# Kernel tuning notes

Measured on AMD Instinct MI355X. Metric: run time of the kernel, lower is better.

## Reference

```python
import jax, jax.numpy as jnp
import numpy as np
from jax import lax

B, CHI, CHO, H, W = 8, 128, 128, 64, 64
K = 3
KK = K * K


def setup_inputs() -> dict:
    key = jax.random.key(0)
    ks = jax.random.split(key, 7)
    x = jax.random.normal(ks[0], (B, CHI, H, W), jnp.float32)
    # small offset-conv weights so sampled offsets stay in a realistic few-pixel range
    off_w = jax.random.normal(ks[1], (3 * KK, CHI, K, K), jnp.float32) * 0.01
    off_b = jnp.zeros((3 * KK,), jnp.float32)
    w = jax.random.normal(ks[2], (CHO, CHI, K, K), jnp.float32) / np.sqrt(CHI * KK).astype(np.float32)
    b = jnp.zeros((CHO,), jnp.float32)
    gamma = jax.random.uniform(ks[3], (CHO,), jnp.float32)  # nn.init.uniform_ on BN weight
    beta = jnp.zeros((CHO,), jnp.float32)
    return {"x": x, "off_w": off_w, "off_b": off_b, "w": w, "b": b, "gamma": gamma, "beta": beta}


def _deform_conv(x, off_w, off_b, w, b):
    """DCNv2 modulated deformable conv, k=3, stride=1, pad=1, dil=1, 1 deform group."""
    B_, C, H_, W_ = x.shape
    # offset/mask branch: plain 3x3 conv -> 27 channels (2*9 offsets, 9 masks)
    om = lax.conv_general_dilated(x, off_w, (1, 1), ((1, 1), (1, 1)),
                                  dimension_numbers=("NCHW", "OIHW", "NCHW"))
    om = om + off_b[None, :, None, None]
    off = om[:, : 2 * KK].reshape(B_, KK, 2, H_, W_)  # [B,9,2,H,W]; ch 2k=y, 2k+1=x
    mask = jax.nn.sigmoid(om[:, 2 * KK:])             # [B,9,H,W]

    ky, kx = jnp.meshgrid(jnp.arange(K, dtype=jnp.float32),
                          jnp.arange(K, dtype=jnp.float32), indexing="ij")
    ky = ky.reshape(KK); kx = kx.reshape(KK)
    # sampling positions: p = p0 - pad + k*dil + offset
    py = off[:, :, 0] + (jnp.arange(H_, dtype=jnp.float32) - 1.0)[None, None, :, None] + ky[None, :, None, None]
    px = off[:, :, 1] + (jnp.arange(W_, dtype=jnp.float32) - 1.0)[None, None, None, :] + kx[None, :, None, None]

    y0 = jnp.floor(py); x0 = jnp.floor(px)
    ly = py - y0; lx = px - x0
    xf = x.reshape(B_, C, H_ * W_)

    def corner(yi, xi, wgt):
        valid = ((yi >= 0) & (yi <= H_ - 1) & (xi >= 0) & (xi <= W_ - 1)).astype(x.dtype)
        yc = jnp.clip(yi, 0, H_ - 1).astype(jnp.int32)
        xc = jnp.clip(xi, 0, W_ - 1).astype(jnp.int32)
        idx = (yc * W_ + xc).reshape(B_, KK * H_ * W_)
        g = jax.vmap(lambda xb, ib: xb[:, ib])(xf, idx).reshape(B_, C, KK, H_, W_)
        return g * (valid * wgt)[:, None]

    val = (corner(y0, x0, (1 - ly) * (1 - lx))
           + corner(y0, x0 + 1, (1 - ly) * lx)
           + corner(y0 + 1, x0, ly * (1 - lx))
           + corner(y0 + 1, x0 + 1, ly * lx))  # [B,C,9,H,W]
    val = val * mask[:, None]  # modulation
    out = jnp.einsum("bckhw,ock->bohw", val, w.reshape(w.shape[0], C, KK))
    return out + b[None, :, None, None]


def reference(x, off_w, off_b, w, b, gamma, beta):
    y = _deform_conv(x, off_w, off_b, w, b)
    # BatchNorm2d in training mode (batch statistics), eps=1e-5, then ReLU
    mean = y.mean(axis=(0, 2, 3))
    var = y.var(axis=(0, 2, 3))
    yn = (y - mean[None, :, None, None]) * lax.rsqrt(var[None, :, None, None] + 1e-5)
    return jax.nn.relu(yn * gamma[None, :, None, None] + beta[None, :, None, None])
```

## Files before the change

### kernel.cpp

```cpp
#include <hip/hip_runtime.h>
#include <hip/hip_bf16.h>
#include <math.h>

#define HH 64
#define WW 64
#define HW 4096
#define LDV 136

typedef __bf16 bf16x8 __attribute__((ext_vector_type(8)));
typedef float floatx4 __attribute__((ext_vector_type(4)));
typedef unsigned int uint4a __attribute__((ext_vector_type(4)));
typedef unsigned int uint2a __attribute__((ext_vector_type(2)));

#define WS_Y    0u
#define WS_PSQ  16777216u
#define WS_XTB  16778240u
#define WS_WTB  25166848u
#define WS_OWB  25461760u

static __device__ inline ushort f2bf(float f) {
  __hip_bfloat16 h = __float2bfloat16(f);
  return __builtin_bit_cast(ushort, h);
}
static __device__ inline float lo16(unsigned int u) { return __builtin_bit_cast(float, u << 16); }
static __device__ inline float hi16(unsigned int u) { return __builtin_bit_cast(float, u & 0xffff0000u); }

static __device__ inline void barrier_lds() {
  asm volatile("s_waitcnt lgkmcnt(0)" ::: "memory");
  __builtin_amdgcn_s_barrier();
}

__global__ __launch_bounds__(256) void k_prep(const float* __restrict__ x,
                                              const float* __restrict__ w,
                                              const float* __restrict__ ow,
                                              ushort* __restrict__ xtb,
                                              ushort* __restrict__ wtb,
                                              ushort* __restrict__ owb,
                                              float* __restrict__ psq) {
  __shared__ float tile[32][33];
  int bid = blockIdx.x;
  if (bid < 4096) {
    int hw0 = (bid & 127) * 32;
    int c0 = ((bid >> 7) & 3) * 32;
    int b = bid >> 9;
    int col = threadIdx.x & 31, row = threadIdx.x >> 5;
    const float* xb = x + ((size_t)b * 128 + c0) * HW + hw0;
#pragma unroll
    for (int i = 0; i < 32; i += 8)
      tile[row + i][col] = xb[(size_t)(row + i) * HW + col];
    __syncthreads();
    int hw = threadIdx.x >> 3, cq = threadIdx.x & 7;
    ushort* xo = xtb + ((size_t)b * HW + hw0) * 128 + c0;
    unsigned int lo = (unsigned int)f2bf(tile[cq * 4 + 0][hw]) |
                      ((unsigned int)f2bf(tile[cq * 4 + 1][hw]) << 16);
    unsigned int hi = (unsigned int)f2bf(tile[cq * 4 + 2][hw]) |
                      ((unsigned int)f2bf(tile[cq * 4 + 3][hw]) << 16);
    uint2a v2 = (uint2a){lo, hi};
    *(uint2a*)(&xo[(size_t)hw * 128 + cq * 4]) = v2;
  } else if (bid < 4096 + 576) {
    int idx = (bid - 4096) * 256 + threadIdx.x;
    int c = idx & 127, o = (idx >> 7) & 127, k = idx >> 14;
    wtb[idx] = f2bf(w[(o * 128 + c) * 9 + k]);
  } else if (bid < 4096 + 720) {
    int j = (bid - 4672) * 256 + threadIdx.x;
    int c = j & 127, o = (j >> 7) & 31, k = j >> 12;
    float v = (o < 27) ? ow[(o * 128 + c) * 9 + k] : 0.f;
    owb[j] = f2bf(v);
  } else {
    psq[threadIdx.x] = 0.f;
  }
}

__global__ __launch_bounds__(256) void k_main(
    const ushort* __restrict__ xtb, const ushort* __restrict__ wtb,
    const ushort* __restrict__ owb, const float* __restrict__ off_b,
    const float* __restrict__ bias, float* __restrict__ y) {
  __shared__ ushort Vl[2][32 * LDV];
  __shared__ float omL[27 * 32];
  int t = threadIdx.x;
  int lane = t & 63, wv = t >> 6;
  int li = lane & 15, quad = lane >> 4;
  int hr = blockIdx.x;
  int row = hr >> 1, p0b = (hr & 1) * 32;
  int b = blockIdx.y;
  const ushort* xb = xtb + (size_t)b * HW * 128;
  int ch = t & 15;
  int pq = t >> 4;

  int mi = wv & 1, ni = wv >> 1;
  floatx4 oacc = (floatx4){0.f, 0.f, 0.f, 0.f};
  uint4a u0, u1;
  auto p1load = [&](int k, int p, uint4a& u) {
    int ky = k / 3, kx = k % 3;
    int ry = row - 1 + ky, cx = p0b + p - 1 + kx;
    bool v = (ry >= 0 && ry < HH && cx >= 0 && cx < WW);
    int idx = v ? (ry * WW + cx) : 0;
    uint4a a = *(const uint4a*)(xb + (size_t)idx * 128 + ch * 8);
    u = v ? a : (uint4a){0u, 0u, 0u, 0u};
  };
  p1load(0, pq, u0);
  p1load(0, pq + 16, u1);
  for (int k = 0; k < 9; ++k) {
    *(uint4a*)(&Vl[k & 1][pq * LDV + ch * 8]) = u0;
    *(uint4a*)(&Vl[k & 1][(pq + 16) * LDV + ch * 8]) = u1;
    if (k < 8) {
      p1load(k + 1, pq, u0);
      p1load(k + 1, pq + 16, u1);
    }
    barrier_lds();
#pragma unroll
    for (int ks = 0; ks < 4; ++ks) {
      bf16x8 bfrag = __builtin_bit_cast(bf16x8,
          *(const uint4a*)(&Vl[k & 1][(ni * 16 + li) * LDV + ks * 32 + quad * 8]));
      bf16x8 afrag = __builtin_bit_cast(bf16x8,
          *(const uint4a*)(&owb[(size_t)(k * 32 + mi * 16 + li) * 128 + ks * 32 + quad * 8]));
      oacc = __builtin_amdgcn_mfma_f32_16x16x32_bf16(afrag, bfrag, oacc, 0, 0, 0);
    }
  }
#pragma unroll
  for (int r = 0; r < 4; ++r) {
    int o = mi * 16 + quad * 4 + r;
    if (o < 27) omL[o * 32 + ni * 16 + li] = oacc[r] + off_b[o];
  }
  __syncthreads();

  floatx4 macc[2][2];
#pragma unroll
  for (int i = 0; i < 2; ++i)
#pragma unroll
    for (int j = 0; j < 2; ++j) macc[i][j] = (floatx4){0.f, 0.f, 0.f, 0.f};

  float wqA[4], wqB[4];
  int idxA[4], idxB[4];
  uint4a u[8];

  auto prep = [&](int k, int p, float* wq, int* idx4) {
    int ky = k / 3, kx = k % 3;
    float offy = omL[(2 * k) * 32 + p];
    float offx = omL[(2 * k + 1) * 32 + p];
    float mraw = omL[(18 + k) * 32 + p];
    float m = 1.f / (1.f + __expf(-mraw));
    float py = offy + (float)(row - 1 + ky);
    float px = offx + (float)(p0b + p - 1 + kx);
    float y0f = floorf(py), x0f = floorf(px);
    float ly = py - y0f, lx = px - x0f;
    int iy0 = (int)y0f, ix0 = (int)x0f;
    int iy1 = iy0 + 1, ix1 = ix0 + 1;
    float w00 = (1.f - ly) * (1.f - lx) * m, w01 = (1.f - ly) * lx * m;
    float w10 = ly * (1.f - lx) * m, w11 = ly * lx * m;
    if (iy0 < 0 || iy0 > HH - 1) { w00 = 0.f; w01 = 0.f; }
    if (iy1 < 0 || iy1 > HH - 1) { w10 = 0.f; w11 = 0.f; }
    if (ix0 < 0 || ix0 > WW - 1) { w00 = 0.f; w10 = 0.f; }
    if (ix1 < 0 || ix1 > WW - 1) { w01 = 0.f; w11 = 0.f; }
    int cy0 = min(max(iy0, 0), HH - 1), cy1 = min(max(iy1, 0), HH - 1);
    int cx0 = min(max(ix0, 0), WW - 1), cx1 = min(max(ix1, 0), WW - 1);
    idx4[0] = cy0 * WW + cx0;
    idx4[1] = cy0 * WW + cx1;
    idx4[2] = cy1 * WW + cx0;
    idx4[3] = cy1 * WW + cx1;
    wq[0] = w00; wq[1] = w01; wq[2] = w10; wq[3] = w11;
  };
  auto issue = [&]() {
#pragma unroll
    for (int c = 0; c < 4; ++c)
      u[c] = *(const uint4a*)(xb + (size_t)idxA[c] * 128 + ch * 8);
#pragma unroll
    for (int c = 0; c < 4; ++c)
      u[4 + c] = *(const uint4a*)(xb + (size_t)idxB[c] * 128 + ch * 8);
  };

  prep(0, pq, wqA, idxA);
  prep(0, pq + 16, wqB, idxB);
  issue();
  for (int k = 0; k < 9; ++k) {
    {
      uint4a outv;
#pragma unroll
      for (int e = 0; e < 4; ++e) {
        float rlo = wqA[0] * lo16(u[0][e]) + wqA[1] * lo16(u[1][e]) +
                    wqA[2] * lo16(u[2][e]) + wqA[3] * lo16(u[3][e]);
        float rhi = wqA[0] * hi16(u[0][e]) + wqA[1] * hi16(u[1][e]) +
                    wqA[2] * hi16(u[2][e]) + wqA[3] * hi16(u[3][e]);
        outv[e] = (unsigned int)f2bf(rlo) | ((unsigned int)f2bf(rhi) << 16);
      }
      *(uint4a*)(&Vl[k & 1][pq * LDV + ch * 8]) = outv;
    }
    {
      uint4a outv;
#pragma unroll
      for (int e = 0; e < 4; ++e) {
        float rlo = wqB[0] * lo16(u[4][e]) + wqB[1] * lo16(u[5][e]) +
                    wqB[2] * lo16(u[6][e]) + wqB[3] * lo16(u[7][e]);
        float rhi = wqB[0] * hi16(u[4][e]) + wqB[1] * hi16(u[5][e]) +
                    wqB[2] * hi16(u[6][e]) + wqB[3] * hi16(u[7][e]);
        outv[e] = (unsigned int)f2bf(rlo) | ((unsigned int)f2bf(rhi) << 16);
      }
      *(uint4a*)(&Vl[k & 1][(pq + 16) * LDV + ch * 8]) = outv;
    }
    if (k < 8) {
      prep(k + 1, pq, wqA, idxA);
      prep(k + 1, pq + 16, wqB, idxB);
      issue();
    }
    barrier_lds();
    const ushort* Arow = &wtb[(size_t)(k * 128 + wv * 32) * 128];
#pragma unroll
    for (int ks = 0; ks < 4; ++ks) {
      bf16x8 b0 = __builtin_bit_cast(bf16x8,
          *(const uint4a*)(&Vl[k & 1][(li)*LDV + ks * 32 + quad * 8]));
      bf16x8 b1 = __builtin_bit_cast(bf16x8,
          *(const uint4a*)(&Vl[k & 1][(16 + li) * LDV + ks * 32 + quad * 8]));
      bf16x8 a0 = __builtin_bit_cast(bf16x8,
          *(const uint4a*)(Arow + (size_t)(li)*128 + ks * 32 + quad * 8));
      bf16x8 a1 = __builtin_bit_cast(bf16x8,
          *(const uint4a*)(Arow + (size_t)(16 + li) * 128 + ks * 32 + quad * 8));
      macc[0][0] = __builtin_amdgcn_mfma_f32_16x16x32_bf16(a0, b0, macc[0][0], 0, 0, 0);
      macc[0][1] = __builtin_amdgcn_mfma_f32_16x16x32_bf16(a0, b1, macc[0][1], 0, 0, 0);
      macc[1][0] = __builtin_amdgcn_mfma_f32_16x16x32_bf16(a1, b0, macc[1][0], 0, 0, 0);
      macc[1][1] = __builtin_amdgcn_mfma_f32_16x16x32_bf16(a1, b1, macc[1][1], 0, 0, 0);
    }
  }
#pragma unroll
  for (int ot = 0; ot < 2; ++ot)
#pragma unroll
    for (int pt = 0; pt < 2; ++pt)
#pragma unroll
      for (int r = 0; r < 4; ++r) {
        int o = wv * 32 + ot * 16 + quad * 4 + r;
        int p = p0b + pt * 16 + li;
        y[((size_t)(b * 128 + o)) * HW + row * 64 + p] = macc[ot][pt][r] + bias[o];
      }
}

__global__ __launch_bounds__(256) void k_stats(const float* __restrict__ y,
                                               float* __restrict__ psq) {
  int o = blockIdx.x, b = blockIdx.y, t = threadIdx.x;
  const float4* yb = (const float4*)(y + ((size_t)(b * 128 + o)) * HW);
  float s = 0.f, q = 0.f;
#pragma unroll
  for (int i = 0; i < 4; ++i) {
    float4 v = yb[t + i * 256];
    s += v.x + v.y + v.z + v.w;
    q += v.x * v.x + v.y * v.y + v.z * v.z + v.w * v.w;
  }
#pragma unroll
  for (int off = 32; off >= 1; off >>= 1) {
    s += __shfl_down(s, off, 64);
    q += __shfl_down(q, off, 64);
  }
  __shared__ float bs[4], bq[4];
  if ((t & 63) == 0) { bs[t >> 6] = s; bq[t >> 6] = q; }
  __syncthreads();
  if (t == 0) {
    atomicAdd(&psq[o], bs[0] + bs[1] + bs[2] + bs[3]);
    atomicAdd(&psq[128 + o], bq[0] + bq[1] + bq[2] + bq[3]);
  }
}

__global__ __launch_bounds__(256) void k_norm(const float* __restrict__ y,
                                              const float* __restrict__ psq,
                                              const float* __restrict__ gamma,
                                              const float* __restrict__ beta,
                                              float* __restrict__ out) {
  int blk = blockIdx.x;
  int o = (blk >> 2) & 127;
  float s = psq[o], q = psq[128 + o];
  float mean = s * (1.f / 32768.f);
  float var = q * (1.f / 32768.f) - mean * mean;
  float scale = gamma[o] * rsqrtf(var + 1e-5f);
  float shift = beta[o] - mean * scale;
  int i4 = blk * 256 + threadIdx.x;
  float4 v = ((const float4*)y)[i4];
  float4 r;
  r.x = fmaxf(v.x * scale + shift, 0.f);
  r.y = fmaxf(v.y * scale + shift, 0.f);
  r.z = fmaxf(v.z * scale + shift, 0.f);
  r.w = fmaxf(v.w * scale + shift, 0.f);
  ((float4*)out)[i4] = r;
}

extern "C" void kernel_launch(void* const* d_in, const int* in_sizes, int n_in,
                              void* d_out, int out_size, void* d_ws, size_t ws_size,
                              hipStream_t stream) {
  const float* x     = (const float*)d_in[0];
  const float* off_w = (const float*)d_in[1];
  const float* off_b = (const float*)d_in[2];
  const float* w     = (const float*)d_in[3];
  const float* bias  = (const float*)d_in[4];
  const float* gamma = (const float*)d_in[5];
  const float* beta  = (const float*)d_in[6];
  float* out = (float*)d_out;
  char* ws = (char*)d_ws;

  float* y    = (float*)(ws + WS_Y);
  float* psq  = (float*)(ws + WS_PSQ);
  ushort* xtb = (ushort*)(ws + WS_XTB);
  ushort* wtb = (ushort*)(ws + WS_WTB);
  ushort* owb = (ushort*)(ws + WS_OWB);

  k_prep<<<4817, 256, 0, stream>>>(x, w, off_w, xtb, wtb, owb, psq);
  k_main<<<dim3(128, 8), 256, 0, stream>>>(xtb, wtb, owb, off_b, bias, y);
  k_stats<<<dim3(128, 8), 256, 0, stream>>>(y, psq);
  k_norm<<<4096, 256, 0, stream>>>(y, psq, gamma, beta, out);
}
```

Measured before the change: 157.2 us.

## Fuse BN statistics into main conv kernel and halve pixel tile per block

Each k_main block now covers 16 pixels instead of 32, which doubles the grid to 2048 blocks for better occupancy and spread across CUs. BN sum and sum-of-squares are computed in the main kernel's epilogue with shuffle reductions and atomics into 8 slotted partial buffers, so the separate k_stats pass that reread y is gone. k_norm sums the 8 slots. The cost is more atomics and redundant offset-conv work per pixel, since half the waves idle during the offset GEMM and weight reuse across pixels halves.

Measured after the change: 185.3 us. 1.18x slower.

```diff
diff --git a/kernel.cpp b/kernel.cpp
--- a/kernel.cpp
+++ b/kernel.cpp
@@ -13,10 +13,10 @@
 typedef unsigned int uint2a __attribute__((ext_vector_type(2)));
 
 #define WS_Y    0u
-#define WS_PSQ  16777216u
-#define WS_XTB  16778240u
-#define WS_WTB  25166848u
-#define WS_OWB  25461760u
+#define WS_XTB  16777216u
+#define WS_WTB  25165824u
+#define WS_OWB  25460736u
+#define WS_PSQ  25534464u
 
 static __device__ inline ushort f2bf(float f) {
   __hip_bfloat16 h = __float2bfloat16(f);
@@ -67,81 +67,79 @@
     float v = (o < 27) ? ow[(o * 128 + c) * 9 + k] : 0.f;
     owb[j] = f2bf(v);
   } else {
-    psq[threadIdx.x] = 0.f;
+    for (int i = threadIdx.x; i < 2048; i += 256) psq[i] = 0.f;
   }
 }
 
 __global__ __launch_bounds__(256) void k_main(
     const ushort* __restrict__ xtb, const ushort* __restrict__ wtb,
     const ushort* __restrict__ owb, const float* __restrict__ off_b,
-    const float* __restrict__ bias, float* __restrict__ y) {
-  __shared__ ushort Vl[2][32 * LDV];
-  __shared__ float omL[27 * 32];
+    const float* __restrict__ bias, float* __restrict__ y,
+    float* __restrict__ psq) {
+  __shared__ ushort Vl[2][16 * LDV];
+  __shared__ float omL[27 * 16];
   int t = threadIdx.x;
   int lane = t & 63, wv = t >> 6;
   int li = lane & 15, quad = lane >> 4;
-  int hr = blockIdx.x;
-  int row = hr >> 1, p0b = (hr & 1) * 32;
+  int bx = blockIdx.x;
+  int row = bx >> 2, p0b = (bx & 3) * 16;
   int b = blockIdx.y;
   const ushort* xb = xtb + (size_t)b * HW * 128;
   int ch = t & 15;
   int pq = t >> 4;
 
-  int mi = wv & 1, ni = wv >> 1;
+  int mi = wv;
   floatx4 oacc = (floatx4){0.f, 0.f, 0.f, 0.f};
-  uint4a u0, u1;
-  auto p1load = [&](int k, int p, uint4a& u) {
+  uint4a u0;
+  auto p1load = [&](int k, uint4a& u) {
     int ky = k / 3, kx = k % 3;
-    int ry = row - 1 + ky, cx = p0b + p - 1 + kx;
+    int ry = row - 1 + ky, cx = p0b + pq - 1 + kx;
     bool v = (ry >= 0 && ry < HH && cx >= 0 && cx < WW);
     int idx = v ? (ry * WW + cx) : 0;
     uint4a a = *(const uint4a*)(xb + (size_t)idx * 128 + ch * 8);
     u = v ? a : (uint4a){0u, 0u, 0u, 0u};
   };
-  p1load(0, pq, u0);
-  p1load(0, pq + 16, u1);
+  p1load(0, u0);
   for (int k = 0; k < 9; ++k) {
     *(uint4a*)(&Vl[k & 1][pq * LDV + ch * 8]) = u0;
-    *(uint4a*)(&Vl[k & 1][(pq + 16) * LDV + ch * 8]) = u1;
-    if (k < 8) {
-      p1load(k + 1, pq, u0);
-      p1load(k + 1, pq + 16, u1);
-    }
+    if (k < 8) p1load(k + 1, u0);
     barrier_lds();
-#pragma unroll
-    for (int ks = 0; ks < 4; ++ks) {
-      bf16x8 bfrag = __builtin_bit_cast(bf16x8,
-          *(const uint4a*)(&Vl[k & 1][(ni * 16 + li) * LDV + ks * 32 + quad * 8]));
-      bf16x8 afrag = __builtin_bit_cast(bf16x8,
-          *(const uint4a*)(&owb[(size_t)(k * 32 + mi * 16 + li) * 128 + ks * 32 + quad * 8]));
-      oacc = __builtin_amdgcn_mfma_f32_16x16x32_bf16(afrag, bfrag, oacc, 0, 0, 0);
-    }
-  }
-#pragma unroll
-  for (int r = 0; r < 4; ++r) {
-    int o = mi * 16 + quad * 4 + r;
-    if (o < 27) omL[o * 32 + ni * 16 + li] = oacc[r] + off_b[o];
+    if (wv < 2) {
+#pragma unroll
+      for (int ks = 0; ks < 4; ++ks) {
+        bf16x8 bfrag = __builtin_bit_cast(bf16x8,
+            *(const uint4a*)(&Vl[k & 1][li * LDV + ks * 32 + quad * 8]));
+        bf16x8 afrag = __builtin_bit_cast(bf16x8,
+            *(const uint4a*)(&owb[(size_t)(k * 32 + mi * 16 + li) * 128 + ks * 32 + quad * 8]));
+        oacc = __builtin_amdgcn_mfma_f32_16x16x32_bf16(afrag, bfrag, oacc, 0, 0, 0);
+      }
+    }
+  }
+  if (wv < 2) {
+#pragma unroll
+    for (int r = 0; r < 4; ++r) {
+      int o = mi * 16 + quad * 4 + r;
+      if (o < 27) omL[o * 16 + li] = oacc[r] + off_b[o];
+    }
   }
   __syncthreads();
 
-  floatx4 macc[2][2];
-#pragma unroll
-  for (int i = 0; i < 2; ++i)
-#pragma unroll
-    for (int j = 0; j < 2; ++j) macc[i][j] = (floatx4){0.f, 0.f, 0.f, 0.f};
-
-  float wqA[4], wqB[4];
-  int idxA[4], idxB[4];
-  uint4a u[8];
-
-  auto prep = [&](int k, int p, float* wq, int* idx4) {
+  floatx4 macc[2];
+#pragma unroll
+  for (int i = 0; i < 2; ++i) macc[i] = (floatx4){0.f, 0.f, 0.f, 0.f};
+
+  float wq[4];
+  int idx4[4];
+  uint4a u[4];
+
+  auto prep = [&](int k) {
     int ky = k / 3, kx = k % 3;
-    float offy = omL[(2 * k) * 32 + p];
-    float offx = omL[(2 * k + 1) * 32 + p];
-    float mraw = omL[(18 + k) * 32 + p];
+    float offy = omL[(2 * k) * 16 + pq];
+    float offx = omL[(2 * k + 1) * 16 + pq];
+    float mraw = omL[(18 + k) * 16 + pq];
     float m = 1.f / (1.f + __expf(-mraw));
     float py = offy + (float)(row - 1 + ky);
-    float px = offx + (float)(p0b + p - 1 + kx);
+    float px = offx + (float)(p0b + pq - 1 + kx);
     float y0f = floorf(py), x0f = floorf(px);
     float ly = py - y0f, lx = px - x0f;
     int iy0 = (int)y0f, ix0 = (int)x0f;
@@ -163,43 +161,26 @@
   auto issue = [&]() {
 #pragma unroll
     for (int c = 0; c < 4; ++c)
-      u[c] = *(const uint4a*)(xb + (size_t)idxA[c] * 128 + ch * 8);
-#pragma unroll
-    for (int c = 0; c < 4; ++c)
-      u[4 + c] = *(const uint4a*)(xb + (size_t)idxB[c] * 128 + ch * 8);
+      u[c] = *(const uint4a*)(xb + (size_t)idx4[c] * 128 + ch * 8);
   };
 
-  prep(0, pq, wqA, idxA);
-  prep(0, pq + 16, wqB, idxB);
+  prep(0);
   issue();
   for (int k = 0; k < 9; ++k) {
     {
       uint4a outv;
 #pragma unroll
       for (int e = 0; e < 4; ++e) {
-        float rlo = wqA[0] * lo16(u[0][e]) + wqA[1] * lo16(u[1][e]) +
-                    wqA[2] * lo16(u[2][e]) + wqA[3] * lo16(u[3][e]);
-        float rhi = wqA[0] * hi16(u[0][e]) + wqA[1] * hi16(u[1][e]) +
-                    wqA[2] * hi16(u[2][e]) + wqA[3] * hi16(u[3][e]);
+        float rlo = wq[0] * lo16(u[0][e]) + wq[1] * lo16(u[1][e]) +
+                    wq[2] * lo16(u[2][e]) + wq[3] * lo16(u[3][e]);
+        float rhi = wq[0] * hi16(u[0][e]) + wq[1] * hi16(u[1][e]) +
+                    wq[2] * hi16(u[2][e]) + wq[3] * hi16(u[3][e]);
         outv[e] = (unsigned int)f2bf(rlo) | ((unsigned int)f2bf(rhi) << 16);
       }
       *(uint4a*)(&Vl[k & 1][pq * LDV + ch * 8]) = outv;
     }
-    {
-      uint4a outv;
-#pragma unroll
-      for (int e = 0; e < 4; ++e) {
-        float rlo = wqB[0] * lo16(u[4][e]) + wqB[1] * lo16(u[5][e]) +
-                    wqB[2] * lo16(u[6][e]) + wqB[3] * lo16(u[7][e]);
-        float rhi = wqB[0] * hi16(u[4][e]) + wqB[1] * hi16(u[5][e]) +
-                    wqB[2] * hi16(u[6][e]) + wqB[3] * hi16(u[7][e]);
-        outv[e] = (unsigned int)f2bf(rlo) | ((unsigned int)f2bf(rhi) << 16);
-      }
-      *(uint4a*)(&Vl[k & 1][(pq + 16) * LDV + ch * 8]) = outv;
-    }
     if (k < 8) {
-      prep(k + 1, pq, wqA, idxA);
-      prep(k + 1, pq + 16, wqB, idxB);
+      prep(k + 1);
       issue();
     }
     barrier_lds();
@@ -207,54 +188,35 @@
 #pragma unroll
     for (int ks = 0; ks < 4; ++ks) {
       bf16x8 b0 = __builtin_bit_cast(bf16x8,
-          *(const uint4a*)(&Vl[k & 1][(li)*LDV + ks * 32 + quad * 8]));
-      bf16x8 b1 = __builtin_bit_cast(bf16x8,
-          *(const uint4a*)(&Vl[k & 1][(16 + li) * LDV + ks * 32 + quad * 8]));
+          *(const uint4a*)(&Vl[k & 1][li * LDV + ks * 32 + quad * 8]));
       bf16x8 a0 = __builtin_bit_cast(bf16x8,
           *(const uint4a*)(Arow + (size_t)(li)*128 + ks * 32 + quad * 8));
       bf16x8 a1 = __builtin_bit_cast(bf16x8,
           *(const uint4a*)(Arow + (size_t)(16 + li) * 128 + ks * 32 + quad * 8));
-      macc[0][0] = __builtin_amdgcn_mfma_f32_16x16x32_bf16(a0, b0, macc[0][0], 0, 0, 0);
-      macc[0][1] = __builtin_amdgcn_mfma_f32_16x16x32_bf16(a0, b1, macc[0][1], 0, 0, 0);
-      macc[1][0] = __builtin_amdgcn_mfma_f32_16x16x32_bf16(a1, b0, macc[1][0], 0, 0, 0);
-      macc[1][1] = __builtin_amdgcn_mfma_f32_16x16x32_bf16(a1, b1, macc[1][1], 0, 0, 0);
-    }
-  }
+      macc[0] = __builtin_amdgcn_mfma_f32_16x16x32_bf16(a0, b0, macc[0], 0, 0, 0);
+      macc[1] = __builtin_amdgcn_mfma_f32_16x16x32_bf16(a1, b0, macc[1], 0, 0, 0);
+    }
+  }
+
+  int slot = bx & 7;
 #pragma unroll
   for (int ot = 0; ot < 2; ++ot)
 #pragma unroll
-    for (int pt = 0; pt < 2; ++pt)
-#pragma unroll
-      for (int r = 0; r < 4; ++r) {
-        int o = wv * 32 + ot * 16 + quad * 4 + r;
-        int p = p0b + pt * 16 + li;
-        y[((size_t)(b * 128 + o)) * HW + row * 64 + p] = macc[ot][pt][r] + bias[o];
-      }
-}
-
-__global__ __launch_bounds__(256) void k_stats(const float* __restrict__ y,
-                                               float* __restrict__ psq) {
-  int o = blockIdx.x, b = blockIdx.y, t = threadIdx.x;
-  const float4* yb = (const float4*)(y + ((size_t)(b * 128 + o)) * HW);
-  float s = 0.f, q = 0.f;
-#pragma unroll
-  for (int i = 0; i < 4; ++i) {
-    float4 v = yb[t + i * 256];
-    s += v.x + v.y + v.z + v.w;
-    q += v.x * v.x + v.y * v.y + v.z * v.z + v.w * v.w;
-  }
-#pragma unroll
-  for (int off = 32; off >= 1; off >>= 1) {
-    s += __shfl_down(s, off, 64);
-    q += __shfl_down(q, off, 64);
-  }
-  __shared__ float bs[4], bq[4];
-  if ((t & 63) == 0) { bs[t >> 6] = s; bq[t >> 6] = q; }
-  __syncthreads();
-  if (t == 0) {
-    atomicAdd(&psq[o], bs[0] + bs[1] + bs[2] + bs[3]);
-    atomicAdd(&psq[128 + o], bq[0] + bq[1] + bq[2] + bq[3]);
-  }
+    for (int r = 0; r < 4; ++r) {
+      int o = wv * 32 + ot * 16 + quad * 4 + r;
+      float v = macc[ot][r] + bias[o];
+      y[((size_t)(b * 128 + o)) * HW + row * 64 + p0b + li] = v;
+      float s = v, q = v * v;
+#pragma unroll
+      for (int m = 1; m < 16; m <<= 1) {
+        s += __shfl_xor(s, m, 64);
+        q += __shfl_xor(q, m, 64);
+      }
+      if (li == 0) {
+        atomicAdd(&psq[slot * 256 + o], s);
+        atomicAdd(&psq[slot * 256 + 128 + o], q);
+      }
+    }
 }
 
 __global__ __launch_bounds__(256) void k_norm(const float* __restrict__ y,
@@ -264,7 +226,12 @@
                                               float* __restrict__ out) {
   int blk = blockIdx.x;
   int o = (blk >> 2) & 127;
-  float s = psq[o], q = psq[128 + o];
+  float s = 0.f, q = 0.f;
+#pragma unroll
+  for (int j = 0; j < 8; ++j) {
+    s += psq[j * 256 + o];
+    q += psq[j * 256 + 128 + o];
+  }
   float mean = s * (1.f / 32768.f);
   float var = q * (1.f / 32768.f) - mean * mean;
   float scale = gamma[o] * rsqrtf(var + 1e-5f);
@@ -293,13 +260,12 @@
   char* ws = (char*)d_ws;
 
   float* y    = (float*)(ws + WS_Y);
-  float* psq  = (float*)(ws + WS_PSQ);
   ushort* xtb = (ushort*)(ws + WS_XTB);
   ushort* wtb = (ushort*)(ws + WS_WTB);
   ushort* owb = (ushort*)(ws + WS_OWB);
+  float* psq  = (float*)(ws + WS_PSQ);
 
   k_prep<<<4817, 256, 0, stream>>>(x, w, off_w, xtb, wtb, owb, psq);
-  k_main<<<dim3(128, 8), 256, 0, stream>>>(xtb, wtb, owb, off_b, bias, y);
-  k_stats<<<dim3(128, 8), 256, 0, stream>>>(y, psq);
+  k_main<<<dim3(256, 8), 256, 0, stream>>>(xtb, wtb, owb, off_b, bias, y, psq);
   k_norm<<<4096, 256, 0, stream>>>(y, psq, gamma, beta, out);
 }
```
